# Kernel tuning notes

Measured on AMD Instinct MI355X. Metric: run time of the kernel, lower is better.

## Reference

```python
import jax, jax.numpy as jnp
import numpy as np

LAYERS, BLOCKS = 10, 2
RES_C, DIL_C, SKIP_C = 128, 128, 256
IN_C, COND_C, OUT_C = 60, 80, 240
INIT_K, K = 10, 2


def _dilations():
    dils = []
    for b in range(BLOCKS):
        n = LAYERS if b < BLOCKS - 1 else LAYERS - 1
        dils += [2 ** i for i in range(n)]
    return dils  # length = blocks*layers - 1 = 19


def conv1d(x, w, b, dilation=1):
    # x: [B, Cin, T], w: [Cout, Cin, K], VALID padding (no padding, like torch Conv1d default)
    y = jax.lax.conv_general_dilated(
        x, w, window_strides=(1,), padding='VALID',
        rhs_dilation=(dilation,), dimension_numbers=('NCH', 'OIH', 'NCH'))
    return y + b[None, :, None]


def setup_inputs() -> dict:
    key = jax.random.key(0)
    ks = jax.random.split(key, 18)
    L = len(_dilations())
    s = 0.05
    return {
        'input': jax.random.normal(ks[0], (4, IN_C, 6144), dtype=jnp.float32),
        'condition': jax.random.normal(ks[1], (4, COND_C, 1), dtype=jnp.float32),
        'start_w': jax.random.normal(ks[2], (RES_C, IN_C, INIT_K), dtype=jnp.float32) * s,
        'start_b': jax.random.normal(ks[3], (RES_C,), dtype=jnp.float32) * s,
        'dil_w': jax.random.normal(ks[4], (L, 2 * DIL_C, RES_C, K), dtype=jnp.float32) * s,
        'dil_b': jax.random.normal(ks[5], (L, 2 * DIL_C), dtype=jnp.float32) * s,
        'cond_w': jax.random.normal(ks[6], (L, 2 * DIL_C, COND_C, 1), dtype=jnp.float32) * s,
        'cond_b': jax.random.normal(ks[7], (L, 2 * DIL_C), dtype=jnp.float32) * s,
        'res_w': jax.random.normal(ks[8], (L, RES_C, DIL_C, 1), dtype=jnp.float32) * s,
        'res_b': jax.random.normal(ks[9], (L, RES_C), dtype=jnp.float32) * s,
        'skip_w': jax.random.normal(ks[10], (L, SKIP_C, DIL_C, 1), dtype=jnp.float32) * s,
        'skip_b': jax.random.normal(ks[11], (L, SKIP_C), dtype=jnp.float32) * s,
        'end_w': jax.random.normal(ks[12], (OUT_C, SKIP_C, 1), dtype=jnp.float32) * s,
        'end_b': jax.random.normal(ks[13], (OUT_C,), dtype=jnp.float32) * s,
        'cond_end_w': jax.random.normal(ks[14], (SKIP_C, COND_C, 1), dtype=jnp.float32) * s,
        'cond_end_b': jax.random.normal(ks[15], (SKIP_C,), dtype=jnp.float32) * s,
    }


def reference(input, condition, start_w, start_b, dil_w, dil_b, cond_w, cond_b,
              res_w, res_b, skip_w, skip_b, end_w, end_b, cond_end_w, cond_end_b):
    dils = _dilations()
    cvec = condition[:, :, 0]  # [B, cond_c] (condition time dim is 1)
    x = conv1d(input, start_w, start_b)  # [B, R, T - initK + 1]
    skip = None
    for i, d in enumerate(dils):
        residual = x
        dilated = conv1d(x, dil_w[i], dil_b[i], dilation=d)  # [B, 2C, T_i]
        condi = jnp.einsum('oc,bc->bo', cond_w[i, :, :, 0], cvec) + cond_b[i]
        dilated = dilated + condi[:, :, None]  # broadcast over time (expand)
        filt, gate = jnp.split(dilated, 2, axis=1)
        x = jnp.tanh(filt) * jax.nn.sigmoid(gate)  # [B, C, T_i]
        s = conv1d(x, skip_w[i], skip_b[i])  # [B, S, T_i]
        skip = s if skip is None else s + skip[:, :, -s.shape[2]:]
        x = conv1d(x, res_w[i], res_b[i])
        x = x + residual[:, :, -x.shape[2]:]
    cend = jnp.einsum('oc,bc->bo', cond_end_w[:, :, 0], cvec) + cond_end_b
    skip = skip + cend[:, :, None]
    out = conv1d(jnp.tanh(skip), end_w, end_b)  # [B, out_c, T_out]
    return jax.nn.sigmoid(out)  # hparams.type == 2
```

## Files before the change

kernel.cpp:

```cpp
#include <hip/hip_runtime.h>
#include <cstdint>
#include <cstddef>

#define NLAYERS 19
#define NB 4
#define RES_C 128
#define DIL2 256
#define SKIPC 256
#define INC 60
#define CONDC 80
#define OUTC 240
#define T_IN 6144
#define T0LEN 6135
#define T_FIN 4601
#define TILE 64
#define LTILE 32
#define BLK 512
#define ZROWS 4608
#define XB_T 6208
#define NSPLIT 4
#define LPG 5

#define NDIL (NLAYERS*256*256)
#define NSKP (NLAYERS*256*128)
#define NRES (NLAYERS*128*128)
#define NEND (256*256)
#define NSTART (10*128*64)

typedef short bf16x8 __attribute__((ext_vector_type(8)));
typedef float f32x4 __attribute__((ext_vector_type(4)));
typedef unsigned uint32x2 __attribute__((ext_vector_type(2)));

#if __has_builtin(__builtin_amdgcn_exp2f)
#define EXP2F(x) __builtin_amdgcn_exp2f(x)
#else
#define EXP2F(x) exp2f(x)
#endif
#if __has_builtin(__builtin_amdgcn_rcpf)
#define RCPF(x) __builtin_amdgcn_rcpf(x)
#else
#define RCPF(x) (1.0f/(x))
#endif

__device__ __forceinline__ float fexp(float x){ return EXP2F(x * 1.4426950408889634f); }
__device__ __forceinline__ float fsigmoid(float x){ return RCPF(1.0f + fexp(-x)); }
__device__ __forceinline__ float ftanh(float x){ return 1.0f - 2.0f * RCPF(1.0f + fexp(2.0f*x)); }

__device__ __forceinline__ unsigned short f2bf(float f){
  unsigned u = __builtin_bit_cast(unsigned, f);
  u = u + 0x7FFFu + ((u >> 16) & 1u);
  return (unsigned short)(u >> 16);
}
__device__ __forceinline__ float bf2f(unsigned short h){
  unsigned u = ((unsigned)h) << 16;
  return __builtin_bit_cast(float, u);
}

__device__ __forceinline__ void gl_lds16(const void* g, void* l){
  __builtin_amdgcn_global_load_lds((const __attribute__((address_space(1))) unsigned int*)g,
                                   (__attribute__((address_space(3))) unsigned int*)l, 16, 0, 0);
}

__global__ void prep_weights(const float* __restrict__ dil_w, const float* __restrict__ skip_w,
                             const float* __restrict__ res_w, const float* __restrict__ end_w,
                             const float* __restrict__ start_w,
                             unsigned short* __restrict__ dilWb, unsigned short* __restrict__ skipWb,
                             unsigned short* __restrict__ resWb, unsigned short* __restrict__ endWb,
                             unsigned short* __restrict__ startWb){
  const int total = NDIL + NSKP + NRES + NEND + NSTART;
  for (int idx = blockIdx.x*256 + threadIdx.x; idx < total; idx += gridDim.x*256){
    if (idx < NDIL){
      int l = idx >> 16; int rem = idx & 65535; int m = rem >> 8; int k = rem & 255;
      int o = ((m & 1) << 7) + (m >> 1); int c = k & 127; int tap = k >> 7;
      dilWb[idx] = f2bf(dil_w[(((size_t)l*256 + o)*128 + c)*2 + tap]);
    } else if (idx < NDIL + NSKP){
      int j = idx - NDIL;
      skipWb[j] = f2bf(skip_w[j]);
    } else if (idx < NDIL + NSKP + NRES){
      int j = idx - NDIL - NSKP;
      resWb[j] = f2bf(res_w[j]);
    } else if (idx < NDIL + NSKP + NRES + NEND){
      int j = idx - NDIL - NSKP - NRES;
      int m = j >> 8; int k = j & 255;
      endWb[j] = (m < OUTC) ? f2bf(end_w[(size_t)m*256 + k]) : 0;
    } else {
      int j = idx - NDIL - NSKP - NRES - NEND;
      int k = j >> 13; int rem = j & 8191; int oc = rem >> 6; int c = rem & 63;
      startWb[j] = (c < INC) ? f2bf(start_w[((size_t)oc*INC + c)*10 + k]) : 0;
    }
  }
}

__global__ void prep_bias(const float* __restrict__ cond, const float* __restrict__ dil_b,
                          const float* __restrict__ cond_w, const float* __restrict__ cond_b,
                          const float* __restrict__ cend_w, const float* __restrict__ cend_b,
                          const float* __restrict__ skip_b,
                          float* __restrict__ cbias, float* __restrict__ sbc){
  int blk = blockIdx.x; int m = threadIdx.x;
  if (blk < NLAYERS*NB){
    int l = blk >> 2, b = blk & 3;
    int o = ((m & 1) << 7) + (m >> 1);
    float acc = dil_b[l*256 + o] + cond_b[l*256 + o];
    const float* w = cond_w + ((size_t)l*256 + o)*CONDC;
    const float* cv = cond + b*CONDC;
    for (int c = 0; c < CONDC; ++c) acc += w[c]*cv[c];
    cbias[((size_t)l*NB + b)*256 + m] = acc;
  } else {
    int b = blk - NLAYERS*NB;
    float acc = cend_b[m];
    const float* w = cend_w + (size_t)m*CONDC;
    const float* cv = cond + b*CONDC;
    for (int c = 0; c < CONDC; ++c) acc += w[c]*cv[c];
    for (int l = 0; l < NLAYERS; ++l) acc += skip_b[l*256 + m];
    sbc[b*256 + m] = acc;
  }
}

__global__ __launch_bounds__(BLK) void start_mfma(const float* __restrict__ in,
    const unsigned short* __restrict__ startWb, const float* __restrict__ bias,
    unsigned short* __restrict__ xb){
  __shared__ char Bs[80*128];
  const int tid = threadIdx.x;
  const int b = blockIdx.y; const int t0 = blockIdx.x * TILE;
  const int lane = tid & 63;
  const int wave = __builtin_amdgcn_readfirstlane(tid >> 6);
  const int q = lane >> 4, r16 = lane & 15;

  #pragma unroll
  for (int i = 0; i < 5; ++i){
    int j = tid + i*BLK;
    int c2 = j / 80, tt = j % 80;
    int c = 2*c2; int gt = t0 + tt;
    float v0 = 0.f, v1 = 0.f;
    if (gt < T_IN && c < INC){
      const float* base = in + ((size_t)(b*INC + c))*T_IN + gt;
      v0 = base[0]; v1 = base[T_IN];
    }
    unsigned u = (unsigned)f2bf(v0) | ((unsigned)f2bf(v1) << 16);
    int slot = c2 >> 2;
    *(unsigned*)(Bs + tt*128 + ((((slot ^ (tt & 7)) << 4)) | ((4*c2) & 15))) = u;
  }
  __syncthreads();

  f32x4 acc[4] = {};
  for (int k = 0; k < 10; ++k){
    const unsigned short* A = startWb + ((size_t)k*128 + wave*16)*64;
    #pragma unroll
    for (int kk = 0; kk < 2; ++kk){
      int k0 = kk*32 + q*8;
      bf16x8 a = *(const bf16x8*)(A + (size_t)r16*64 + k0);
      int slot = k0 >> 3;
      #pragma unroll
      for (int nt = 0; nt < 4; ++nt){
        int t = nt*16 + r16 + k;
        bf16x8 bf = *(const bf16x8*)(Bs + t*128 + ((slot ^ (t & 7)) << 4));
        acc[nt] = __builtin_amdgcn_mfma_f32_16x16x32_bf16(a, bf, acc[nt], 0, 0, 0);
      }
    }
  }
  const float* bb = bias + wave*16;
  #pragma unroll
  for (int nt = 0; nt < 4; ++nt){
    int gt = t0 + nt*16 + r16;
    if (gt < T0LEN){
      float v[4];
      #pragma unroll
      for (int rr = 0; rr < 4; ++rr) v[rr] = acc[nt][rr] + bb[4*q + rr];
      uint32x2 u;
      u.x = (unsigned)f2bf(v[0]) | ((unsigned)f2bf(v[1]) << 16);
      u.y = (unsigned)f2bf(v[2]) | ((unsigned)f2bf(v[3]) << 16);
      *(uint32x2*)(xb + ((size_t)b*XB_T + gt)*128 + wave*16 + 4*q) = u;
    }
  }
}

__global__ __launch_bounds__(BLK) void layer_mfma(
    const unsigned short* __restrict__ xbin, unsigned short* __restrict__ xbout,
    unsigned short* __restrict__ zl,
    const unsigned short* __restrict__ dilWb, const unsigned short* __restrict__ resWb,
    const float* __restrict__ cbias, const float* __restrict__ res_b,
    int layer, int d, int Tin, int Tout, int woff, int last){
  __shared__ char BxT0[LTILE*256];
  __shared__ char BxT1[LTILE*256];
  __shared__ char Bz[LTILE*256];
  const int tid = threadIdx.x;
  const int b = blockIdx.y; const int t0 = blockIdx.x*LTILE;
  const int lane = tid & 63;
  const int wave = __builtin_amdgcn_readfirstlane(tid >> 6);
  const int q = lane >> 4;
  const int r16 = lane & 15;

  {
    int r = lane >> 4;
    int p = lane & 15;
    int row0 = wave*4;
    int trow = row0 + r;
    int so = (p ^ (trow & 15)) * 8;
    const unsigned short* gb = xbin + (size_t)b*XB_T*128;
    gl_lds16(gb + (size_t)(t0 + trow)*128 + so,     BxT0 + row0*256);
    gl_lds16(gb + (size_t)(t0 + trow + d)*128 + so, BxT1 + row0*256);
  }
  __syncthreads();

  f32x4 acc[2][2] = {};
  #pragma unroll
  for (int tap = 0; tap < 2; ++tap){
    const char* Bt = tap ? BxT1 : BxT0;
    const unsigned short* A = dilWb + (size_t)layer*256*256 + (size_t)(wave*32)*256 + tap*128;
    for (int kk = 0; kk < 4; ++kk){
      int k0 = kk*32 + q*8;
      bf16x8 a0 = *(const bf16x8*)(A + (size_t)r16*256 + k0);
      bf16x8 a1 = *(const bf16x8*)(A + (size_t)(16 + r16)*256 + k0);
      int slot = k0 >> 3;
      #pragma unroll
      for (int nt = 0; nt < 2; ++nt){
        int t = nt*16 + r16;
        bf16x8 bf = *(const bf16x8*)(Bt + t*256 + ((slot ^ (t & 15)) << 4));
        acc[0][nt] = __builtin_amdgcn_mfma_f32_16x16x32_bf16(a0, bf, acc[0][nt], 0, 0, 0);
        acc[1][nt] = __builtin_amdgcn_mfma_f32_16x16x32_bf16(a1, bf, acc[1][nt], 0, 0, 0);
      }
    }
  }

  {
    const float* cb = cbias + ((size_t)layer*NB + b)*256 + wave*32;
    #pragma unroll
    for (int mt = 0; mt < 2; ++mt){
      float bf0 = cb[mt*16 + 4*q + 0];
      float bg0 = cb[mt*16 + 4*q + 1];
      float bf1 = cb[mt*16 + 4*q + 2];
      float bg1 = cb[mt*16 + 4*q + 3];
      int ch0 = wave*16 + mt*8 + 2*q;
      int slot = ch0 >> 3;
      #pragma unroll
      for (int nt = 0; nt < 2; ++nt){
        float z0 = ftanh(acc[mt][nt][0] + bf0) * fsigmoid(acc[mt][nt][1] + bg0);
        float z1 = ftanh(acc[mt][nt][2] + bf1) * fsigmoid(acc[mt][nt][3] + bg1);
        int t = nt*16 + r16;
        unsigned u = (unsigned)f2bf(z0) | ((unsigned)f2bf(z1) << 16);
        *(unsigned*)(Bz + t*256 + ((slot ^ (t & 15)) << 4) + ((2*ch0) & 15)) = u;
      }
    }
  }
  __syncthreads();

  {
    unsigned short* zgb = zl + (size_t)b*ZROWS*128;
    #pragma unroll
    for (int i = 0; i < 4; ++i){
      int j = tid + i*BLK;
      int row = j >> 6, cu = j & 63;
      int gt = t0 + row;
      int windex = gt - woff;
      if (gt < Tout && windex >= 0){
        int slot = cu >> 2;
        unsigned u = *(const unsigned*)(Bz + row*256 + (((slot ^ (row & 15)) << 4) | ((4*cu) & 15)));
        *(unsigned*)(zgb + (size_t)windex*128 + 2*cu) = u;
      }
    }
  }

  if (!last){
    f32x4 racc[2] = {};
    const unsigned short* A = resWb + (size_t)layer*128*128 + (size_t)(wave*16)*128;
    for (int kk = 0; kk < 4; ++kk){
      int k0 = kk*32 + q*8;
      bf16x8 a0 = *(const bf16x8*)(A + (size_t)r16*128 + k0);
      int slot = k0 >> 3;
      #pragma unroll
      for (int nt = 0; nt < 2; ++nt){
        int t = nt*16 + r16;
        bf16x8 bf = *(const bf16x8*)(Bz + t*256 + ((slot ^ (t & 15)) << 4));
        racc[nt] = __builtin_amdgcn_mfma_f32_16x16x32_bf16(a0, bf, racc[nt], 0, 0, 0);
      }
    }
    const float* rb = res_b + layer*RES_C + wave*16;
    #pragma unroll
    for (int nt = 0; nt < 2; ++nt){
      int t = nt*16 + r16;
      float v[4];
      #pragma unroll
      for (int rr = 0; rr < 4; ++rr){
        int m = wave*16 + 4*q + rr;
        unsigned short xh = *(const unsigned short*)(BxT1 + t*256 +
            ((((m >> 3) ^ (t & 15)) << 4) | ((2*m) & 15)));
        v[rr] = racc[nt][rr] + rb[4*q + rr] + bf2f(xh);
      }
      uint32x2 u;
      u.x = (unsigned)f2bf(v[0]) | ((unsigned)f2bf(v[1]) << 16);
      u.y = (unsigned)f2bf(v[2]) | ((unsigned)f2bf(v[3]) << 16);
      int m0 = wave*16 + 4*q;
      int slot = m0 >> 3;
      *(uint32x2*)(BxT0 + t*256 + (((slot ^ (t & 15)) << 4) | ((2*m0) & 15))) = u;
    }
    __syncthreads();
    unsigned short* xg = xbout + (size_t)b*XB_T*128;
    #pragma unroll
    for (int i = 0; i < 4; ++i){
      int j = tid + i*BLK;
      int row = j >> 6, cu = j & 63;
      int gt = t0 + row;
      if (gt < Tout){
        int slot = cu >> 2;
        unsigned u = *(const unsigned*)(BxT0 + row*256 + (((slot ^ (row & 15)) << 4) | ((4*cu) & 15)));
        *(unsigned*)(xg + (size_t)gt*128 + 2*cu) = u;
      }
    }
  }
}

__global__ __launch_bounds__(BLK) void skipsum_mfma(
    const unsigned short* __restrict__ zbuf,
    const unsigned short* __restrict__ skipWb,
    float* __restrict__ partial){
  __shared__ char BzP[2][64*256];
  const int tid = threadIdx.x;
  const int b = blockIdx.y; const int t0 = blockIdx.x*TILE;
  const int g = blockIdx.z;
  const int l0 = g*LPG;
  const int l1 = (l0 + LPG < NLAYERS) ? (l0 + LPG) : NLAYERS;
  const int lane = tid & 63;
  const int wave = __builtin_amdgcn_readfirstlane(tid >> 6);
  const int q = lane >> 4, r16 = lane & 15;

  auto stageZ = [&](int l, int buf){
    int r = lane >> 4, p = lane & 15;
    const unsigned short* zb = zbuf + ((size_t)l*NB + b)*ZROWS*128;
    #pragma unroll
    for (int h = 0; h < 2; ++h){
      int row0 = wave*8 + h*4;
      int trow = row0 + r;
      gl_lds16(zb + (size_t)(t0 + trow)*128 + (p ^ (trow & 15))*8,
               BzP[buf] + row0*256);
    }
  };

  stageZ(l0, l0 & 1);
  __syncthreads();

  f32x4 sacc[2][4] = {};
  for (int l = l0; l < l1; ++l){
    if (l + 1 < l1) stageZ(l + 1, (l + 1) & 1);
    const unsigned short* A = skipWb + ((size_t)l*256 + wave*32)*128;
    const char* Bb = BzP[l & 1];
    for (int kk = 0; kk < 4; ++kk){
      int k0 = kk*32 + q*8;
      bf16x8 a0 = *(const bf16x8*)(A + (size_t)r16*128 + k0);
      bf16x8 a1 = *(const bf16x8*)(A + (size_t)(16 + r16)*128 + k0);
      int slot = k0 >> 3;
      #pragma unroll
      for (int nt = 0; nt < 4; ++nt){
        int t = nt*16 + r16;
        bf16x8 bf = *(const bf16x8*)(Bb + t*256 + ((slot ^ (t & 15)) << 4));
        sacc[0][nt] = __builtin_amdgcn_mfma_f32_16x16x32_bf16(a0, bf, sacc[0][nt], 0, 0, 0);
        sacc[1][nt] = __builtin_amdgcn_mfma_f32_16x16x32_bf16(a1, bf, sacc[1][nt], 0, 0, 0);
      }
    }
    __syncthreads();
  }

  float* pg = partial + (size_t)g*NB*SKIPC*T_FIN;
  #pragma unroll
  for (int mt = 0; mt < 2; ++mt){
    #pragma unroll
    for (int nt = 0; nt < 4; ++nt){
      int gt = t0 + nt*16 + r16;
      if (gt < T_FIN){
        #pragma unroll
        for (int rr = 0; rr < 4; ++rr){
          int m = wave*32 + mt*16 + 4*q + rr;
          pg[((size_t)(b*SKIPC + m))*T_FIN + gt] = sacc[mt][nt][rr];
        }
      }
    }
  }
}

__global__ __launch_bounds__(BLK) void end_mfma(
    const float* __restrict__ partial, const unsigned short* __restrict__ endWb,
    const float* __restrict__ sbc, const float* __restrict__ end_b,
    float* __restrict__ out){
  __shared__ char Bs[64*512];
  const int tid = threadIdx.x;
  const int b = blockIdx.y; const int t0 = blockIdx.x*TILE;
  const int lane = tid & 63;
  const int wave = __builtin_amdgcn_readfirstlane(tid >> 6);
  const int q = lane >> 4;
  const int r16 = lane & 15;
  const size_t gs = (size_t)NB*SKIPC*T_FIN;

  {
    const int t = lane;
    const int gt = t0 + t;
    #pragma unroll
    for (int i = 0; i < 32; i += 2){
      int s0 = wave*32 + i;
      float v0 = 0.f, v1 = 0.f;
      if (gt < T_FIN){
        size_t base = ((size_t)(b*SKIPC + s0))*T_FIN + gt;
        float a0 = partial[base]        + partial[base + gs]
                 + partial[base + 2*gs] + partial[base + 3*gs];
        float a1 = partial[base + T_FIN]        + partial[base + T_FIN + gs]
                 + partial[base + T_FIN + 2*gs] + partial[base + T_FIN + 3*gs];
        v0 = ftanh(a0 + sbc[b*256 + s0]);
        v1 = ftanh(a1 + sbc[b*256 + s0 + 1]);
      }
      unsigned u = (unsigned)f2bf(v0) | ((unsigned)f2bf(v1) << 16);
      int slot = s0 >> 3;
      *(unsigned*)(Bs + t*512 + ((slot ^ (t & 31)) << 4) + ((2*s0) & 15)) = u;
    }
  }
  __syncthreads();

  f32x4 acc[2][4] = {};
  const unsigned short* A = endWb + (size_t)(wave*32)*256;
  for (int kk = 0; kk < 8; ++kk){
    int k0 = kk*32 + q*8;
    bf16x8 a0 = *(const bf16x8*)(A + (size_t)r16*256 + k0);
    bf16x8 a1 = *(const bf16x8*)(A + (size_t)(16 + r16)*256 + k0);
    int slot = k0 >> 3;
    #pragma unroll
    for (int nt = 0; nt < 4; ++nt){
      int t = nt*16 + r16;
      bf16x8 bf = *(const bf16x8*)(Bs + t*512 + ((slot ^ (t & 31)) << 4));
      acc[0][nt] = __builtin_amdgcn_mfma_f32_16x16x32_bf16(a0, bf, acc[0][nt], 0, 0, 0);
      acc[1][nt] = __builtin_amdgcn_mfma_f32_16x16x32_bf16(a1, bf, acc[1][nt], 0, 0, 0);
    }
  }
  #pragma unroll
  for (int mt = 0; mt < 2; ++mt){
    #pragma unroll
    for (int nt = 0; nt < 4; ++nt){
      int gt = t0 + nt*16 + r16;
      if (gt < T_FIN){
        #pragma unroll
        for (int rr = 0; rr < 4; ++rr){
          int m = wave*32 + mt*16 + 4*q + rr;
          if (m < OUTC)
            out[((size_t)(b*OUTC + m))*T_FIN + gt] = fsigmoid(acc[mt][nt][rr] + end_b[m]);
        }
      }
    }
  }
}

extern "C" void kernel_launch(void* const* d_in, const int* in_sizes, int n_in,
                              void* d_out, int out_size, void* d_ws, size_t ws_size,
                              hipStream_t stream){
  const float* input     = (const float*)d_in[0];
  const float* condition = (const float*)d_in[1];
  const float* start_w   = (const float*)d_in[2];
  const float* start_b   = (const float*)d_in[3];
  const float* dil_w     = (const float*)d_in[4];
  const float* dil_b     = (const float*)d_in[5];
  const float* cond_w    = (const float*)d_in[6];
  const float* cond_b    = (const float*)d_in[7];
  const float* res_w     = (const float*)d_in[8];
  const float* res_b     = (const float*)d_in[9];
  const float* skip_w    = (const float*)d_in[10];
  const float* skip_b    = (const float*)d_in[11];
  const float* end_w     = (const float*)d_in[12];
  const float* end_b     = (const float*)d_in[13];
  const float* cend_w    = (const float*)d_in[14];
  const float* cend_b    = (const float*)d_in[15];
  float* out = (float*)d_out;

  char* ws = (char*)d_ws;
  size_t off = 0;
  auto carve = [&](size_t bytes) -> char* {
    char* p = ws + off; off = (off + bytes + 255) & ~(size_t)255; return p;
  };
  unsigned short* xbA  = (unsigned short*)carve((size_t)NB*XB_T*128*2);
  unsigned short* xbB  = (unsigned short*)carve((size_t)NB*XB_T*128*2);
  unsigned short* zbuf = (unsigned short*)carve((size_t)NLAYERS*NB*ZROWS*128*2);
  float* partial       = (float*)carve((size_t)NSPLIT*NB*SKIPC*T_FIN*4);
  unsigned short* dilWb   = (unsigned short*)carve((size_t)NDIL*2);
  unsigned short* skipWb  = (unsigned short*)carve((size_t)NSKP*2);
  unsigned short* resWb   = (unsigned short*)carve((size_t)NRES*2);
  unsigned short* endWb   = (unsigned short*)carve((size_t)NEND*2);
  unsigned short* startWb = (unsigned short*)carve((size_t)NSTART*2);
  float* cbias = (float*)carve((size_t)NLAYERS*NB*256*4);
  float* sbc   = (float*)carve((size_t)NB*256*4);

  prep_weights<<<2048, 256, 0, stream>>>(dil_w, skip_w, res_w, end_w, start_w,
                                         dilWb, skipWb, resWb, endWb, startWb);
  prep_bias<<<NLAYERS*NB + NB, 256, 0, stream>>>(condition, dil_b, cond_w, cond_b,
                                                 cend_w, cend_b, skip_b, cbias, sbc);

  {
    dim3 grid((T0LEN + TILE - 1)/TILE, NB);
    start_mfma<<<grid, BLK, 0, stream>>>(input, startWb, start_b, xbA);
  }

  int dils[NLAYERS]; int n = 0;
  for (int bb = 0; bb < 2; ++bb){ int nn = (bb==0) ? 10 : 9; for (int k = 0; k < nn; ++k) dils[n++] = 1<<k; }

  unsigned short* xbin = xbA; unsigned short* xbo = xbB;
  int Tin = T0LEN;
  for (int i = 0; i < NLAYERS; ++i){
    int d = dils[i]; int Tout = Tin - d;
    dim3 grid((Tout + LTILE - 1)/LTILE, NB);
    unsigned short* zlp = zbuf + (size_t)i*NB*ZROWS*128;
    layer_mfma<<<grid, BLK, 0, stream>>>(xbin, xbo, zlp, dilWb, resWb,
                                         cbias, res_b, i, d, Tin, Tout,
                                         Tout - T_FIN, (i==NLAYERS-1)?1:0);
    unsigned short* t2 = xbin; xbin = xbo; xbo = t2;
    Tin = Tout;
  }

  {
    dim3 grid((T_FIN + TILE - 1)/TILE, NB, NSPLIT);
    skipsum_mfma<<<grid, BLK, 0, stream>>>(zbuf, skipWb, partial);
  }
  {
    dim3 grid((T_FIN + TILE - 1)/TILE, NB);
    end_mfma<<<grid, BLK, 0, stream>>>(partial, endWb, sbc, end_b, out);
  }
}
```

Before: 486.0 us.

## Store z and residual outputs directly from registers; halve skip-sum layer split

The gated activations and the updated residual tile are now written to global memory straight from the MFMA accumulator registers. Previously they were staged through shared memory and then copied out in a coalesced loop, which needed an extra barrier for the residual tile. The skip-sum kernel now groups 10 layers per block instead of 5, so the end kernel reads and adds two partial buffers instead of four. The trade-off is less coalesced per-lane global stores and fewer blocks available to run the skip-sum stage in parallel.

```diff
diff --git a/kernel.cpp b/kernel.cpp
--- a/kernel.cpp
+++ b/kernel.cpp
@@ -18,8 +18,8 @@
 #define BLK 512
 #define ZROWS 4608
 #define XB_T 6208
-#define NSPLIT 4
-#define LPG 5
+#define NSPLIT 2
+#define LPG 10
 
 #define NDIL (NLAYERS*256*256)
 #define NSKP (NLAYERS*256*128)
@@ -224,6 +224,7 @@
 
   {
     const float* cb = cbias + ((size_t)layer*NB + b)*256 + wave*32;
+    unsigned short* zgb = zl + (size_t)b*ZROWS*128;
     #pragma unroll
     for (int mt = 0; mt < 2; ++mt){
       float bf0 = cb[mt*16 + 4*q + 0];
@@ -239,26 +240,14 @@
         int t = nt*16 + r16;
         unsigned u = (unsigned)f2bf(z0) | ((unsigned)f2bf(z1) << 16);
         *(unsigned*)(Bz + t*256 + ((slot ^ (t & 15)) << 4) + ((2*ch0) & 15)) = u;
+        int gt = t0 + t;
+        int windex = gt - woff;
+        if (gt < Tout && windex >= 0)
+          *(unsigned*)(zgb + (size_t)windex*128 + ch0) = u;
       }
     }
   }
   __syncthreads();
-
-  {
-    unsigned short* zgb = zl + (size_t)b*ZROWS*128;
-    #pragma unroll
-    for (int i = 0; i < 4; ++i){
-      int j = tid + i*BLK;
-      int row = j >> 6, cu = j & 63;
-      int gt = t0 + row;
-      int windex = gt - woff;
-      if (gt < Tout && windex >= 0){
-        int slot = cu >> 2;
-        unsigned u = *(const unsigned*)(Bz + row*256 + (((slot ^ (row & 15)) << 4) | ((4*cu) & 15)));
-        *(unsigned*)(zgb + (size_t)windex*128 + 2*cu) = u;
-      }
-    }
-  }
 
   if (!last){
     f32x4 racc[2] = {};
@@ -275,9 +264,11 @@
       }
     }
     const float* rb = res_b + layer*RES_C + wave*16;
+    unsigned short* xg = xbout + (size_t)b*XB_T*128;
     #pragma unroll
     for (int nt = 0; nt < 2; ++nt){
       int t = nt*16 + r16;
+      int gt = t0 + t;
       float v[4];
       #pragma unroll
       for (int rr = 0; rr < 4; ++rr){
@@ -286,24 +277,11 @@
             ((((m >> 3) ^ (t & 15)) << 4) | ((2*m) & 15)));
         v[rr] = racc[nt][rr] + rb[4*q + rr] + bf2f(xh);
       }
-      uint32x2 u;
-      u.x = (unsigned)f2bf(v[0]) | ((unsigned)f2bf(v[1]) << 16);
-      u.y = (unsigned)f2bf(v[2]) | ((unsigned)f2bf(v[3]) << 16);
-      int m0 = wave*16 + 4*q;
-      int slot = m0 >> 3;
-      *(uint32x2*)(BxT0 + t*256 + (((slot ^ (t & 15)) << 4) | ((2*m0) & 15))) = u;
-    }
-    __syncthreads();
-    unsigned short* xg = xbout + (size_t)b*XB_T*128;
-    #pragma unroll
-    for (int i = 0; i < 4; ++i){
-      int j = tid + i*BLK;
-      int row = j >> 6, cu = j & 63;
-      int gt = t0 + row;
       if (gt < Tout){
-        int slot = cu >> 2;
-        unsigned u = *(const unsigned*)(BxT0 + row*256 + (((slot ^ (row & 15)) << 4) | ((4*cu) & 15)));
-        *(unsigned*)(xg + (size_t)gt*128 + 2*cu) = u;
+        uint32x2 u;
+        u.x = (unsigned)f2bf(v[0]) | ((unsigned)f2bf(v[1]) << 16);
+        u.y = (unsigned)f2bf(v[2]) | ((unsigned)f2bf(v[3]) << 16);
+        *(uint32x2*)(xg + (size_t)gt*128 + wave*16 + 4*q) = u;
       }
     }
   }
@@ -398,10 +376,8 @@
       float v0 = 0.f, v1 = 0.f;
       if (gt < T_FIN){
         size_t base = ((size_t)(b*SKIPC + s0))*T_FIN + gt;
-        float a0 = partial[base]        + partial[base + gs]
-                 + partial[base + 2*gs] + partial[base + 3*gs];
-        float a1 = partial[base + T_FIN]        + partial[base + T_FIN + gs]
-                 + partial[base + T_FIN + 2*gs] + partial[base + T_FIN + 3*gs];
+        float a0 = partial[base]         + partial[base + gs];
+        float a1 = partial[base + T_FIN] + partial[base + T_FIN + gs];
         v0 = ftanh(a0 + sbc[b*256 + s0]);
         v1 = ftanh(a1 + sbc[b*256 + s0 + 1]);
       }
```

Measured after the change: 519.8 us. 7.0% more time.
